# Optimization experiments

Hardware: AMD Instinct MI355X
Metric: run time of the kernel (lower is better)

The kernel has to match this reference:

```python
import jax, jax.numpy as jnp
import numpy as np

COST_CLASS = 1.0
COST_OBJECTNESS = 5.0
COST_GIOU = 2.0
COST_CENTER = 10.0

B, Q, G, C = 32, 1024, 64, 256


def _lsa(cost):
    """Exact rectangular linear sum assignment (Jonker-Volgenant shortest
    augmenting path, same algorithm as scipy.optimize.linear_sum_assignment).
    cost: (R, Cc) float64 numpy array. Returns (row_ind, col_ind), row_ind sorted."""
    transposed = cost.shape[0] > cost.shape[1]
    if transposed:
        cost = cost.T
    n, m = cost.shape
    u = np.zeros(n)
    v = np.zeros(m)
    col4row = np.full(n, -1, dtype=np.int64)
    row4col = np.full(m, -1, dtype=np.int64)
    for cur_row in range(n):
        shortest = np.full(m, np.inf)
        path = np.full(m, -1, dtype=np.int64)
        SC = np.zeros(m, dtype=bool)
        SR_rows = []
        min_val = 0.0
        i = cur_row
        sink = -1
        while sink == -1:
            SR_rows.append(i)
            idx = np.where(~SC)[0]
            r = min_val + cost[i, idx] - u[i] - v[idx]
            better = r < shortest[idx]
            upd = idx[better]
            shortest[upd] = r[better]
            path[upd] = i
            j = idx[np.argmin(shortest[idx])]
            min_val = shortest[j]
            SC[j] = True
            if row4col[j] == -1:
                sink = j
            else:
                i = row4col[j]
        # dual variable update
        u[cur_row] += min_val
        for irow in SR_rows:
            if irow != cur_row:
                u[irow] += min_val - shortest[col4row[irow]]
        v[SC] -= min_val - shortest[SC]
        # augment along the alternating path back to cur_row
        j = sink
        while True:
            i = path[j]
            row4col[j] = i
            col4row[i], j = j, col4row[i]
            if i == cur_row:
                break
    if transposed:
        order = np.argsort(col4row)
        return col4row[order], np.arange(n)[order]
    return np.arange(n), col4row


def setup_inputs() -> dict:
    key = jax.random.key(0)
    k1, k2, k3, k4, k5 = jax.random.split(key, 5)
    return {
        "sem_cls_prob": jax.random.uniform(k1, (B, Q, C), dtype=jnp.float32),
        "objectness_prob": jax.random.uniform(k2, (B, Q), dtype=jnp.float32),
        "center_dist": jax.random.uniform(k3, (B, Q, G), dtype=jnp.float32),
        "gious": jax.random.uniform(k4, (B, Q, G), dtype=jnp.float32),
        "nactual_gt": jax.random.randint(k5, (B,), 0, G, dtype=jnp.int64)
        if jax.config.jax_enable_x64 else jax.random.randint(k5, (B,), 0, G).astype(jnp.int32),
    }


def reference(sem_cls_prob, objectness_prob, center_dist, gious, nactual_gt):
    batchsize, nprop = objectness_prob.shape
    # class_mat == 0 in the original module
    final_cost = (COST_OBJECTNESS * (-objectness_prob[..., None])
                  + COST_CENTER * center_dist
                  + COST_GIOU * (-gious))  # [B, Q, G]
    cost_np = np.asarray(final_cost, dtype=np.float64)
    ngt = np.asarray(nactual_gt)
    per_prop_gt_inds = np.zeros((batchsize, nprop), dtype=np.int64)
    proposal_matched_mask = np.zeros((batchsize, nprop), dtype=np.float32)
    for b in range(batchsize):  # per-batch independent Hungarian (as in source)
        g = int(ngt[b])
        if g > 0:
            rows, cols = _lsa(cost_np[b, :, :g])
            per_prop_gt_inds[b, rows] = cols
            proposal_matched_mask[b, rows] = 1.0
    return jnp.asarray(per_prop_gt_inds), jnp.asarray(proposal_matched_mask)
```

## Files before the change

kernel.cpp:

```cpp
#include <hip/hip_runtime.h>
#include <math.h>

#define B_ 32
#define Q_ 1024
#define G_ 64
#define K16 16

typedef double v16d __attribute__((ext_vector_type(16)));
typedef float  v16f __attribute__((ext_vector_type(16)));
typedef int    v16i __attribute__((ext_vector_type(16)));

#define REP16(OP) OP(0,0) OP(1,1) OP(2,2) OP(3,3) OP(4,4) OP(5,5) OP(6,6) OP(7,7) \
                  OP(8,8) OP(9,9) OP(10,a) OP(11,b) OP(12,c) OP(13,d) OP(14,e) OP(15,f)
#define REP16A(OP,A) OP(A,0,0) OP(A,1,1) OP(A,2,2) OP(A,3,3) OP(A,4,4) OP(A,5,5) OP(A,6,6) OP(A,7,7) \
                     OP(A,8,8) OP(A,9,9) OP(A,10,a) OP(A,11,b) OP(A,12,c) OP(A,13,d) OP(A,14,e) OP(A,15,f)

#define ROR1 0x121
#define ROR2 0x122
#define ROR4 0x124
#define ROR8 0x128
#define BC15 0x142
#define BC31 0x143

template<int CTRL>
__device__ __forceinline__ double dpp_f64(double x) {
    union { double d; int i[2]; } a; a.d = x;
    union { int i[2]; double d; } r;
    r.i[0] = __builtin_amdgcn_update_dpp(a.i[0], a.i[0], CTRL, 0xF, 0xF, false);
    r.i[1] = __builtin_amdgcn_update_dpp(a.i[1], a.i[1], CTRL, 0xF, 0xF, false);
    return r.d;
}
template<int CTRL>
__device__ __forceinline__ int dpp_i32(int x) {
    return __builtin_amdgcn_update_dpp(x, x, CTRL, 0xF, 0xF, false);
}

__device__ __forceinline__ double readlane_f64(double x, int sl) {
    const int s = __builtin_amdgcn_readfirstlane(sl);
    union { double d; int i2[2]; } a; a.d = x;
    union { int i2[2]; double d; } r;
    r.i2[0] = __builtin_amdgcn_readlane(a.i2[0], s);
    r.i2[1] = __builtin_amdgcn_readlane(a.i2[1], s);
    return r.d;
}
__device__ __forceinline__ double readlane_f64c(double x, int sl) {
    union { double d; int i2[2]; } a; a.d = x;
    union { int i2[2]; double d; } r;
    r.i2[0] = __builtin_amdgcn_readlane(a.i2[0], sl);
    r.i2[1] = __builtin_amdgcn_readlane(a.i2[1], sl);
    return r.d;
}
__device__ __forceinline__ float readlane_f32u(float x, int sl) {
    union { float f; int i; } a; a.f = x;
    union { int i; float f; } r;
    r.i = __builtin_amdgcn_readlane(a.i, __builtin_amdgcn_readfirstlane(sl));
    return r.f;
}
__device__ __forceinline__ int readlane_i32(int x, int sl) {
    return __builtin_amdgcn_readlane(x, __builtin_amdgcn_readfirstlane(sl));
}
__device__ __forceinline__ int readlane_i32c(int x, int sl) {
    return __builtin_amdgcn_readlane(x, sl);
}

__device__ __forceinline__ int sel16v(v16i p, int s) {
    const int t0_0 = (s & 1) ? p.s1 : p.s0;
    const int t0_1 = (s & 1) ? p.s3 : p.s2;
    const int t0_2 = (s & 1) ? p.s5 : p.s4;
    const int t0_3 = (s & 1) ? p.s7 : p.s6;
    const int t0_4 = (s & 1) ? p.s9 : p.s8;
    const int t0_5 = (s & 1) ? p.sb : p.sa;
    const int t0_6 = (s & 1) ? p.sd : p.sc;
    const int t0_7 = (s & 1) ? p.sf : p.se;
    const int t1_0 = (s & 2) ? t0_1 : t0_0;
    const int t1_1 = (s & 2) ? t0_3 : t0_2;
    const int t1_2 = (s & 2) ? t0_5 : t0_4;
    const int t1_3 = (s & 2) ? t0_7 : t0_6;
    const int a0 = (s & 4) ? t1_1 : t1_0;
    const int a1 = (s & 4) ? t1_3 : t1_2;
    return (s & 8) ? a1 : a0;
}
__device__ __forceinline__ v16i set_el16(v16i v, int idx, bool cond, int val) {
#define SE16_(K,H) v.s##H = (cond && idx == K) ? val : v.s##H;
    REP16(SE16_)
#undef SE16_
    return v;
}

__device__ __forceinline__ void lexpair(v16d cand, int l,
                                        double& gv_o, int& jm_o) {
    double v = cand.s0; int j = l;
#define LPK_(K,H) if (K > 0) { const bool t = cand.s##H < v; \
    v = t ? cand.s##H : v; j = t ? (l + (K << 6)) : j; }
    REP16(LPK_)
#undef LPK_
#define LP_STEP(C) { const double pv = dpp_f64<C>(v); const int pj = dpp_i32<C>(j); \
    const bool t = (pv < v) || ((pv == v) && (pj < j)); \
    v = t ? pv : v; j = t ? pj : j; }
    LP_STEP(ROR1) LP_STEP(ROR2) LP_STEP(ROR4) LP_STEP(ROR8)
    LP_STEP(BC15) LP_STEP(BC31)
#undef LP_STEP
    gv_o = readlane_f64c(v, 63);
    jm_o = readlane_i32c(j, 63);
}

__global__ __launch_bounds__(256) void build_kernel(
    const float* __restrict__ obj, const float* __restrict__ cd,
    const float* __restrict__ gi, float* __restrict__ ct,
    float* __restrict__ pv, int* __restrict__ pj)
{
    __shared__ float tile[64][65];
    const int b  = blockIdx.y;
    const int jb = blockIdx.x << 6;
    const int t  = threadIdx.x;
    const float* objb = obj + (b << 10);
    const float4* cd4 = (const float4*)(cd + ((size_t)b << 16));
    const float4* gi4 = (const float4*)(gi + ((size_t)b << 16));

    #pragma unroll
    for (int p = 0; p < 4; ++p) {
        const int f  = t + (p << 8);
        const int jj = f >> 4;
        const int q  = f & 15;
        const int i0 = q << 2;
        const int j  = jb + jj;
        const float om = __fmul_rn(5.0f, -objb[j]);
        const float4 c4 = cd4[(j << 4) + q];
        const float4 q4 = gi4[(j << 4) + q];
        tile[i0 + 0][jj] = __fadd_rn(__fadd_rn(om, __fmul_rn(10.0f, c4.x)), __fmul_rn(2.0f, -q4.x));
        tile[i0 + 1][jj] = __fadd_rn(__fadd_rn(om, __fmul_rn(10.0f, c4.y)), __fmul_rn(2.0f, -q4.y));
        tile[i0 + 2][jj] = __fadd_rn(__fadd_rn(om, __fmul_rn(10.0f, c4.z)), __fmul_rn(2.0f, -q4.z));
        tile[i0 + 3][jj] = __fadd_rn(__fadd_rn(om, __fmul_rn(10.0f, c4.w)), __fmul_rn(2.0f, -q4.w));
    }
    __syncthreads();
    #pragma unroll
    for (int r = 0; r < 16; ++r) {
        const int idx = (r << 8) + t;
        const int i = idx >> 6, j2 = idx & 63;
        ct[(((size_t)(b << 6) + i) << 10) + jb + j2] = tile[i][j2];
    }
    if (t < 64) {
        float bv = tile[t][0]; int bc = 0;
        #pragma unroll 8
        for (int c = 1; c < 64; ++c) {
            const float v = tile[t][c];
            if (v < bv) { bv = v; bc = c; }
        }
        const int o = (((b << 6) + t) << 4) + blockIdx.x;
        pv[o] = bv;
        pj[o] = jb + bc;
    }
}

#define LD_W_(D,K,H) D.s##H = rp_[(K) << 6];
#define LD_N_(D,K,H) { const int idx_ = ((l + ((K) << 6)) << 6) + ri_; \
    D.s##H = __fadd_rn(__fadd_rn(objm.s##H, __fmul_rn(10.0f, cdb[idx_])), \
                       __fmul_rn(2.0f, -gib[idx_])); }
#define LOAD_ROW(ri, dst) { const int ri_ = (ri); \
    if (HASWS) { const float* rp_ = ctb + ((size_t)ri_ << 10) + l; REP16A(LD_W_, dst) } \
    else       { REP16A(LD_N_, dst) } }

template<bool HASWS>
__global__ __launch_bounds__(64, 1) void matcher_k(
    const float* __restrict__ obj, const float* __restrict__ cd,
    const float* __restrict__ gi, const int* __restrict__ ngt,
    const float* __restrict__ ct, const float* __restrict__ pv,
    const int* __restrict__ pj, float* __restrict__ out_ind,
    float* __restrict__ out_mask)
{
    const int b = blockIdx.x;
    const int l = threadIdx.x;
    const int g = ngt[b];

    const float* objb = obj + (b << 10);
    const float* cdb  = cd + ((size_t)b << 16);
    const float* gib  = gi + ((size_t)b << 16);
    const float* ctb  = HASWS ? (ct + ((size_t)(b << 6) << 10)) : (const float*)nullptr;

    v16f objm;
    if (!HASWS) {
#define OBJI_(K,H) objm.s##H = __fmul_rn(5.0f, -objb[l + (K << 6)]);
        REP16(OBJI_)
#undef OBJI_
    }

    float pre_v = 0.0f; int pre_j = 0;
    if (HASWS) {
        const float* pvb = pv + (((b << 6) + l) << 4);
        const int*   pjb = pj + (((b << 6) + l) << 4);
        float bv = pvb[0]; int bj = pjb[0];
        #pragma unroll
        for (int q = 1; q < 16; ++q) {
            const float vq = pvb[q];
            const int  jq = pjb[q];
            if (vq < bv) { bv = vq; bj = jq; }
        }
        pre_v = bv; pre_j = bj;
    } else if (g > 0) {
        for (int i = 0; i < g; ++i) {
            v16f c; LOAD_ROW(i, c)
            v16d c64;
#define CV_(K,H) c64.s##H = (double)c.s##H;
            REP16(CV_)
#undef CV_
            double gv; int j0;
            lexpair(c64, l, gv, j0);
            pre_v = (l == i) ? (float)gv : pre_v;
            pre_j = (l == i) ? j0 : pre_j;
        }
    }

    const double INF = __builtin_inf();
    double u_rep = 0.0;
    double m_rec = 0.0;
    bool   inSR  = false;
    int    c4r_rep = -1;
    unsigned asg   = 0u;
    unsigned dirty = 0u;
    v16d v_r, sh_r;
    v16i path, r4c;
    v16f c_cur, c_i;
#define INI_(K,H) { v_r.s##H = 0.0; sh_r.s##H = 0.0; path.s##H = 0; r4c.s##H = -1; }
    REP16(INI_)
#undef INI_

    for (int cur = 0; cur < g; ++cur) {
        double minv = (double)readlane_f32u(pre_v, cur);
        int jm = readlane_i32(pre_j, cur);
        const unsigned dw = (unsigned)readlane_i32((int)dirty, jm & 63);
        bool have_cur = false;
        if ((dw >> (jm >> 6)) & 1u) {
            LOAD_ROW(cur, c_cur) have_cur = true;
            v16d rr0;
#define RR0_(K,H) rr0.s##H = (double)c_cur.s##H - v_r.s##H;
            REP16(RR0_)
#undef RR0_
            lexpair(rr0, l, minv, jm);
        }
        const int owner0 = jm & 63, slot0 = jm >> 6;
        const unsigned oa0 = (unsigned)readlane_i32((int)asg, owner0);

        if (!((oa0 >> slot0) & 1u)) {
            u_rep   = (l == cur)    ? u_rep + minv : u_rep;
            c4r_rep = (l == cur)    ? jm           : c4r_rep;
            asg     = (l == owner0) ? (asg | (1u << slot0)) : asg;
            r4c     = set_el16(r4c, slot0, l == owner0, cur);
        } else {
            if (!have_cur) LOAD_ROW(cur, c_cur)
            int i = readlane_i32(sel16v(r4c, slot0), owner0);
            double ui = readlane_f64(u_rep, i);
            LOAD_ROW(i, c_i)
            unsigned sc = (l == owner0) ? (1u << slot0) : 0u;
            inSR  = (l == i);
            m_rec = minv;
#define SH0_(K,H) { sh_r.s##H = (double)c_cur.s##H - v_r.s##H; path.s##H = cur; }
            REP16(SH0_)
#undef SH0_

            int sink = -1;
            while (sink < 0) {
                v16d cand;
#define DST_(K,H) { const double rr = ((minv + (double)c_i.s##H) - ui) - v_r.s##H; \
                    const bool notSC = !((sc >> K) & 1u); \
                    const bool upd = notSC && (rr < sh_r.s##H);  \
                    sh_r.s##H = upd ? rr : sh_r.s##H; \
                    path.s##H = upd ? i : path.s##H; \
                    cand.s##H = notSC ? sh_r.s##H : INF; }
                REP16(DST_)
#undef DST_
                lexpair(cand, l, minv, jm);
                const int ow = jm & 63, sl = jm >> 6;
                if (l == ow) sc |= (1u << sl);
                const int insp = readlane_i32(sel16v(r4c, sl), ow);
                const unsigned oa = (unsigned)readlane_i32((int)asg, ow);
                if (!((oa >> sl) & 1u)) {
                    sink = jm;
                } else {
                    i = insp;
                    if (l == i) { inSR = true; m_rec = minv; }
                    ui = readlane_f64(u_rep, i);
                    LOAD_ROW(i, c_i)
                }
            }

            if (l == cur)       u_rep += minv;
            else if (inSR)      u_rep += minv - m_rec;
#define VUP_(K,H) { const double nv = v_r.s##H - (minv - sh_r.s##H); \
                    v_r.s##H = ((sc >> K) & 1u) ? nv : v_r.s##H; }
            REP16(VUP_)
#undef VUP_
            dirty |= sc;

            int j = sink;
            while (true) {
                const int so = j & 63, ss = j >> 6;
                const int ii = readlane_i32(sel16v(path, ss), so);
                const int nj = readlane_i32(c4r_rep, ii);
                r4c     = set_el16(r4c, ss, l == so, ii);
                asg     = (l == so) ? (asg | (1u << ss)) : asg;
                c4r_rep = (l == ii) ? j : c4r_rep;
                j = nj;
                if (ii == cur) break;
            }
        }
    }

#define OUT_(K,H) { const int rc = r4c.s##H; const int jj = l + (K << 6); \
    out_ind [(b << 10) + jj] = (rc >= 0) ? (float)rc : 0.0f; \
    out_mask[(b << 10) + jj] = (rc >= 0) ? 1.0f : 0.0f; }
    REP16(OUT_)
#undef OUT_
}

extern "C" void kernel_launch(void* const* d_in, const int* in_sizes, int n_in,
                              void* d_out, int out_size, void* d_ws, size_t ws_size,
                              hipStream_t stream)
{
    const float* obj = (const float*)d_in[1];
    const float* cd  = (const float*)d_in[2];
    const float* gi  = (const float*)d_in[3];
    const int*   ngt = (const int*)d_in[4];
    float* out0 = (float*)d_out;
    float* out1 = out0 + B_ * Q_;

    const size_t ct_b = (size_t)B_ * G_ * Q_ * sizeof(float);
    const size_t pv_b = (size_t)B_ * G_ * 16 * sizeof(float);
    if (ws_size >= ct_b + 2 * pv_b) {
        float* ct = (float*)d_ws;
        float* pv = (float*)((char*)d_ws + ct_b);
        int*   pj = (int*)((char*)d_ws + ct_b + pv_b);
        build_kernel<<<dim3(16, B_), 256, 0, stream>>>(obj, cd, gi, ct, pv, pj);
        matcher_k<true><<<B_, 64, 0, stream>>>(obj, cd, gi, ngt, ct, pv, pj, out0, out1);
    } else {
        matcher_k<false><<<B_, 64, 0, stream>>>(obj, cd, gi, ngt,
                                                nullptr, nullptr, nullptr, out0, out1);
    }
}
```

Measured before the change: 177.4 us.

## Add second-best column precompute, ballot-based assignment lookup, and cheaper argmin reduction

The build kernel now also tracks the second-smallest cost per row, and the matcher merges both. When the best column has been modified, the second-best is used to skip reloading and rescanning the row, as long as it is still clean. The dirty mask now only marks columns whose dual actually changed. The r4c vector is removed in favour of a wave ballot over col4row. Lexpair is rewritten as a value-only DPP min followed by a packed-key index min, which shortens the reduction chain on every Dijkstra step. The risks are subtle correctness issues in tie-breaking and the second-best shortcut, plus extra workspace traffic.

```diff
diff --git a/kernel.cpp b/kernel.cpp
--- a/kernel.cpp
+++ b/kernel.cpp
@@ -63,7 +63,7 @@
     return __builtin_amdgcn_readlane(x, sl);
 }
 
-__device__ __forceinline__ int sel16v(v16i p, int s) {
+__device__ __forceinline__ int sel16v_i(v16i p, int s) {
     const int t0_0 = (s & 1) ? p.s1 : p.s0;
     const int t0_1 = (s & 1) ? p.s3 : p.s2;
     const int t0_2 = (s & 1) ? p.s5 : p.s4;
@@ -80,34 +80,61 @@
     const int a1 = (s & 4) ? t1_3 : t1_2;
     return (s & 8) ? a1 : a0;
 }
-__device__ __forceinline__ v16i set_el16(v16i v, int idx, bool cond, int val) {
-#define SE16_(K,H) v.s##H = (cond && idx == K) ? val : v.s##H;
-    REP16(SE16_)
-#undef SE16_
-    return v;
-}
-
-__device__ __forceinline__ void lexpair(v16d cand, int l,
+__device__ __forceinline__ double sel16v_d(v16d p, int s) {
+    const double t0_0 = (s & 1) ? p.s1 : p.s0;
+    const double t0_1 = (s & 1) ? p.s3 : p.s2;
+    const double t0_2 = (s & 1) ? p.s5 : p.s4;
+    const double t0_3 = (s & 1) ? p.s7 : p.s6;
+    const double t0_4 = (s & 1) ? p.s9 : p.s8;
+    const double t0_5 = (s & 1) ? p.sb : p.sa;
+    const double t0_6 = (s & 1) ? p.sd : p.sc;
+    const double t0_7 = (s & 1) ? p.sf : p.se;
+    const double t1_0 = (s & 2) ? t0_1 : t0_0;
+    const double t1_1 = (s & 2) ? t0_3 : t0_2;
+    const double t1_2 = (s & 2) ? t0_5 : t0_4;
+    const double t1_3 = (s & 2) ? t0_7 : t0_6;
+    const double a0 = (s & 4) ? t1_1 : t1_0;
+    const double a1 = (s & 4) ? t1_3 : t1_2;
+    return (s & 8) ? a1 : a0;
+}
+
+__device__ __forceinline__ void lexpair(v16d c, int l,
                                         double& gv_o, int& jm_o) {
-    double v = cand.s0; int j = l;
-#define LPK_(K,H) if (K > 0) { const bool t = cand.s##H < v; \
-    v = t ? cand.s##H : v; j = t ? (l + (K << 6)) : j; }
-    REP16(LPK_)
-#undef LPK_
-#define LP_STEP(C) { const double pv = dpp_f64<C>(v); const int pj = dpp_i32<C>(j); \
-    const bool t = (pv < v) || ((pv == v) && (pj < j)); \
-    v = t ? pv : v; j = t ? pj : j; }
-    LP_STEP(ROR1) LP_STEP(ROR2) LP_STEP(ROR4) LP_STEP(ROR8)
-    LP_STEP(BC15) LP_STEP(BC31)
-#undef LP_STEP
-    gv_o = readlane_f64c(v, 63);
-    jm_o = readlane_i32c(j, 63);
+    const double a0 = fmin(c.s0, c.s1), a1 = fmin(c.s2, c.s3),
+                 a2 = fmin(c.s4, c.s5), a3 = fmin(c.s6, c.s7),
+                 a4 = fmin(c.s8, c.s9), a5 = fmin(c.sa, c.sb),
+                 a6 = fmin(c.sc, c.sd), a7 = fmin(c.se, c.sf);
+    const double b0 = fmin(a0, a1), b1 = fmin(a2, a3),
+                 b2 = fmin(a4, a5), b3 = fmin(a6, a7);
+    const double d0 = fmin(b0, b1), d1 = fmin(b2, b3);
+    const double vloc = fmin(d0, d1);
+    double v = vloc;
+#define VS_(C) { const double pv = dpp_f64<C>(v); v = fmin(pv, v); }
+    VS_(ROR1) VS_(ROR2) VS_(ROR4) VS_(ROR8) VS_(BC15) VS_(BC31)
+#undef VS_
+    const double gv = readlane_f64c(v, 63);
+    const int bit3 = (d0 == gv) ? 0 : 1;
+    const double bsel = bit3 ? b2 : b0;
+    const int bit2 = (bsel == gv) ? 0 : 1;
+    const double asel = bit2 ? (bit3 ? a6 : a2) : (bit3 ? a4 : a0);
+    const int bit1 = (asel == gv) ? 0 : 1;
+    const double csel = bit1 ? (bit2 ? (bit3 ? c.se : c.s6) : (bit3 ? c.sa : c.s2))
+                             : (bit2 ? (bit3 ? c.sc : c.s4) : (bit3 ? c.s8 : c.s0));
+    const int bit0 = (csel == gv) ? 0 : 1;
+    const int kloc = (bit3 << 3) | (bit2 << 2) | (bit1 << 1) | bit0;
+    int key = (vloc == gv) ? ((kloc << 6) | l) : 0x7FFFFFFF;
+#define KS_(C) { const int pk = dpp_i32<C>(key); key = (pk < key) ? pk : key; }
+    KS_(ROR1) KS_(ROR2) KS_(ROR4) KS_(ROR8) KS_(BC15) KS_(BC31)
+#undef KS_
+    jm_o = readlane_i32c(key, 63);
+    gv_o = gv;
 }
 
 __global__ __launch_bounds__(256) void build_kernel(
     const float* __restrict__ obj, const float* __restrict__ cd,
     const float* __restrict__ gi, float* __restrict__ ct,
-    float* __restrict__ pv, int* __restrict__ pj)
+    float* __restrict__ pv, int* __restrict__ pj,
+    float* __restrict__ pv2, int* __restrict__ pj2)
 {
     __shared__ float tile[64][65];
     const int b  = blockIdx.y;
@@ -141,14 +168,20 @@
     }
     if (t < 64) {
         float bv = tile[t][0]; int bc = 0;
+        float sv = 1e30f;      int sc2 = 0;
         #pragma unroll 8
         for (int c = 1; c < 64; ++c) {
             const float v = tile[t][c];
-            if (v < bv) { bv = v; bc = c; }
+            const bool t1 = v < bv;
+            const bool t2 = (!t1) && (v < sv);
+            sv  = t1 ? bv : (t2 ? v : sv);
+            sc2 = t1 ? bc : (t2 ? c : sc2);
+            bv  = t1 ? v : bv;
+            bc  = t1 ? c : bc;
         }
         const int o = (((b << 6) + t) << 4) + blockIdx.x;
-        pv[o] = bv;
-        pj[o] = jb + bc;
+        pv[o]  = bv;  pj[o]  = jb + bc;
+        pv2[o] = sv;  pj2[o] = jb + sc2;
     }
 }
 
@@ -165,7 +198,8 @@
     const float* __restrict__ obj, const float* __restrict__ cd,
     const float* __restrict__ gi, const int* __restrict__ ngt,
     const float* __restrict__ ct, const float* __restrict__ pv,
-    const int* __restrict__ pj, float* __restrict__ out_ind,
+    const int* __restrict__ pj, const float* __restrict__ pv2,
+    const int* __restrict__ pj2, float* __restrict__ out_ind,
     float* __restrict__ out_mask)
 {
     const int b = blockIdx.x;
@@ -184,18 +218,29 @@
 #undef OBJI_
     }
 
-    float pre_v = 0.0f; int pre_j = 0;
+    float pre_v = 0.0f, sec_v = 0.0f; int pre_j = 0, sec_j = 0;
     if (HASWS) {
-        const float* pvb = pv + (((b << 6) + l) << 4);
-        const int*   pjb = pj + (((b << 6) + l) << 4);
-        float bv = pvb[0]; int bj = pjb[0];
-        #pragma unroll
-        for (int q = 1; q < 16; ++q) {
-            const float vq = pvb[q];
-            const int  jq = pjb[q];
-            if (vq < bv) { bv = vq; bj = jq; }
-        }
-        pre_v = bv; pre_j = bj;
+        const int base = ((b << 6) + l) << 4;
+        const float4* pvq = (const float4*)(pv  + base);
+        const int4*   pjq = (const int4*)(pj  + base);
+        const float4* svq = (const float4*)(pv2 + base);
+        const int4*   sjq = (const int4*)(pj2 + base);
+        const float4 pA = pvq[0], pB = pvq[1], pC = pvq[2], pD = pvq[3];
+        const int4   jA = pjq[0], jB = pjq[1], jC = pjq[2], jD = pjq[3];
+        const float4 sA = svq[0], sB = svq[1], sC = svq[2], sD = svq[3];
+        const int4   tA = sjq[0], tB = sjq[1], tC = sjq[2], tD = sjq[3];
+        float bv = pA.x; int bj = jA.x; float sv = sA.x; int sj = tA.x;
+#define MERGE_(CV,CJ,C2V,C2J) { const bool nb = (CV) < bv; \
+    const bool s1 = (C2V) < bv; const bool s2 = (CV) < sv; \
+    const float nsv = nb ? (s1 ? (C2V) : bv) : (s2 ? (CV) : sv); \
+    const int   nsj = nb ? (s1 ? (C2J) : bj) : (s2 ? (CJ) : sj); \
+    bj = nb ? (CJ) : bj; bv = nb ? (CV) : bv; sv = nsv; sj = nsj; }
+        MERGE_(pA.y,jA.y,sA.y,tA.y) MERGE_(pA.z,jA.z,sA.z,tA.z) MERGE_(pA.w,jA.w,sA.w,tA.w)
+        MERGE_(pB.x,jB.x,sB.x,tB.x) MERGE_(pB.y,jB.y,sB.y,tB.y) MERGE_(pB.z,jB.z,sB.z,tB.z) MERGE_(pB.w,jB.w,sB.w,tB.w)
+        MERGE_(pC.x,jC.x,sC.x,tC.x) MERGE_(pC.y,jC.y,sC.y,tC.y) MERGE_(pC.z,jC.z,sC.z,tC.z) MERGE_(pC.w,jC.w,sC.w,tC.w)
+        MERGE_(pD.x,jD.x,sD.x,tD.x) MERGE_(pD.y,jD.y,sD.y,tD.y) MERGE_(pD.z,jD.z,sD.z,tD.z) MERGE_(pD.w,jD.w,sD.w,tD.w)
+#undef MERGE_
+        pre_v = bv; pre_j = bj; sec_v = sv; sec_j = sj;
     } else if (g > 0) {
         for (int i = 0; i < g; ++i) {
             v16f c; LOAD_ROW(i, c)
@@ -208,6 +253,7 @@
             pre_v = (l == i) ? (float)gv : pre_v;
             pre_j = (l == i) ? j0 : pre_j;
         }
+        sec_v = pre_v; sec_j = pre_j;
     }
 
     const double INF = __builtin_inf();
@@ -218,39 +264,53 @@
     unsigned asg   = 0u;
     unsigned dirty = 0u;
     v16d v_r, sh_r;
-    v16i path, r4c;
+    v16i path;
     v16f c_cur, c_i;
-#define INI_(K,H) { v_r.s##H = 0.0; sh_r.s##H = 0.0; path.s##H = 0; r4c.s##H = -1; }
+#define INI_(K,H) { v_r.s##H = 0.0; sh_r.s##H = 0.0; path.s##H = 0; }
     REP16(INI_)
 #undef INI_
 
     for (int cur = 0; cur < g; ++cur) {
-        double minv = (double)readlane_f32u(pre_v, cur);
+        const float pre_vc = readlane_f32u(pre_v, cur);
         int jm = readlane_i32(pre_j, cur);
-        const unsigned dw = (unsigned)readlane_i32((int)dirty, jm & 63);
+        double minv = (double)pre_vc;
         bool have_cur = false;
-        if ((dw >> (jm >> 6)) & 1u) {
-            LOAD_ROW(cur, c_cur) have_cur = true;
-            v16d rr0;
+        {
+            const int ow1 = jm & 63, sl1 = jm >> 6;
+            const unsigned d1 = (unsigned)readlane_i32((int)dirty, ow1);
+            if ((d1 >> sl1) & 1u) {
+                const float sv_c = readlane_f32u(sec_v, cur);
+                const int   sj_c = readlane_i32(sec_j, cur);
+                const unsigned d2 = (unsigned)readlane_i32((int)dirty, sj_c & 63);
+                if (!((d2 >> (sj_c >> 6)) & 1u)) {
+                    const double vpj = readlane_f64(sel16v_d(v_r, sl1), ow1);
+                    const double vA = (double)pre_vc - vpj;
+                    const double vB = (double)sv_c;
+                    const bool t = (vB < vA) || ((vB == vA) && (sj_c < jm));
+                    minv = t ? vB : vA;
+                    jm   = t ? sj_c : jm;
+                } else {
+                    LOAD_ROW(cur, c_cur) have_cur = true;
+                    v16d rr0;
 #define RR0_(K,H) rr0.s##H = (double)c_cur.s##H - v_r.s##H;
-            REP16(RR0_)
+                    REP16(RR0_)
 #undef RR0_
-            lexpair(rr0, l, minv, jm);
+                    lexpair(rr0, l, minv, jm);
+                }
+            }
         }
-        const int owner0 = jm & 63, slot0 = jm >> 6;
-        const unsigned oa0 = (unsigned)readlane_i32((int)asg, owner0);
-
-        if (!((oa0 >> slot0) & 1u)) {
-            u_rep   = (l == cur)    ? u_rep + minv : u_rep;
-            c4r_rep = (l == cur)    ? jm           : c4r_rep;
-            asg     = (l == owner0) ? (asg | (1u << slot0)) : asg;
-            r4c     = set_el16(r4c, slot0, l == owner0, cur);
+        const unsigned long long mk0 = __ballot(c4r_rep == jm);
+
+        if (mk0 == 0ull) {
+            u_rep   = (l == cur) ? u_rep + minv : u_rep;
+            c4r_rep = (l == cur) ? jm           : c4r_rep;
+            asg     = (l == (jm & 63)) ? (asg | (1u << (jm >> 6))) : asg;
         } else {
             if (!have_cur) LOAD_ROW(cur, c_cur)
-            int i = readlane_i32(sel16v(r4c, slot0), owner0);
+            int i = (int)__builtin_ctzll(mk0);
+            LOAD_ROW(i, c_i)
             double ui = readlane_f64(u_rep, i);
-            LOAD_ROW(i, c_i)
-            unsigned sc = (l == owner0) ? (1u << slot0) : 0u;
+            unsigned sc = (l == (jm & 63)) ? (1u << (jm >> 6)) : 0u;
             inSR  = (l == i);
             m_rec = minv;
 #define SH0_(K,H) { sh_r.s##H = (double)c_cur.s##H - v_r.s##H; path.s##H = cur; }
@@ -269,34 +329,34 @@
                 REP16(DST_)
 #undef DST_
                 lexpair(cand, l, minv, jm);
-                const int ow = jm & 63, sl = jm >> 6;
-                if (l == ow) sc |= (1u << sl);
-                const int insp = readlane_i32(sel16v(r4c, sl), ow);
-                const unsigned oa = (unsigned)readlane_i32((int)asg, ow);
-                if (!((oa >> sl) & 1u)) {
+                const unsigned long long mk = __ballot(c4r_rep == jm);
+                if (l == (jm & 63)) sc |= (1u << (jm >> 6));
+                if (mk == 0ull) {
                     sink = jm;
                 } else {
-                    i = insp;
+                    i = (int)__builtin_ctzll(mk);
+                    LOAD_ROW(i, c_i)
                     if (l == i) { inSR = true; m_rec = minv; }
                     ui = readlane_f64(u_rep, i);
-                    LOAD_ROW(i, c_i)
                 }
             }
 
             if (l == cur)       u_rep += minv;
             else if (inSR)      u_rep += minv - m_rec;
-#define VUP_(K,H) { const double nv = v_r.s##H - (minv - sh_r.s##H); \
-                    v_r.s##H = ((sc >> K) & 1u) ? nv : v_r.s##H; }
+            unsigned chg = 0u;
+#define VUP_(K,H) { const bool in_sc = (sc >> K) & 1u; \
+                    const double nv = v_r.s##H - (minv - sh_r.s##H); \
+                    chg = (in_sc && (sh_r.s##H != minv)) ? (chg | (1u << K)) : chg; \
+                    v_r.s##H = in_sc ? nv : v_r.s##H; }
             REP16(VUP_)
 #undef VUP_
-            dirty |= sc;
+            dirty |= chg;
 
             int j = sink;
             while (true) {
                 const int so = j & 63, ss = j >> 6;
-                const int ii = readlane_i32(sel16v(path, ss), so);
+                const int ii = readlane_i32(sel16v_i(path, ss), so);
                 const int nj = readlane_i32(c4r_rep, ii);
-                r4c     = set_el16(r4c, ss, l == so, ii);
                 asg     = (l == so) ? (asg | (1u << ss)) : asg;
                 c4r_rep = (l == ii) ? j : c4r_rep;
                 j = nj;
@@ -305,11 +365,12 @@
         }
     }
 
-#define OUT_(K,H) { const int rc = r4c.s##H; const int jj = l + (K << 6); \
-    out_ind [(b << 10) + jj] = (rc >= 0) ? (float)rc : 0.0f; \
-    out_mask[(b << 10) + jj] = (rc >= 0) ? 1.0f : 0.0f; }
+#define OUT_(K,H) { const int jj = l + (K << 6); const bool a_ = (asg >> K) & 1u; \
+    out_mask[(b << 10) + jj] = a_ ? 1.0f : 0.0f; \
+    if (!a_) out_ind[(b << 10) + jj] = 0.0f; }
     REP16(OUT_)
 #undef OUT_
+    if (c4r_rep >= 0) out_ind[(b << 10) + c4r_rep] = (float)l;
 }
 
 extern "C" void kernel_launch(void* const* d_in, const int* in_sizes, int n_in,
@@ -325,14 +386,17 @@
 
     const size_t ct_b = (size_t)B_ * G_ * Q_ * sizeof(float);
     const size_t pv_b = (size_t)B_ * G_ * 16 * sizeof(float);
-    if (ws_size >= ct_b + 2 * pv_b) {
-        float* ct = (float*)d_ws;
-        float* pv = (float*)((char*)d_ws + ct_b);
-        int*   pj = (int*)((char*)d_ws + ct_b + pv_b);
-        build_kernel<<<dim3(16, B_), 256, 0, stream>>>(obj, cd, gi, ct, pv, pj);
-        matcher_k<true><<<B_, 64, 0, stream>>>(obj, cd, gi, ngt, ct, pv, pj, out0, out1);
+    if (ws_size >= ct_b + 4 * pv_b) {
+        float* ct  = (float*)d_ws;
+        float* pv  = (float*)((char*)d_ws + ct_b);
+        int*   pj  = (int*)  ((char*)d_ws + ct_b + pv_b);
+        float* pv2 = (float*)((char*)d_ws + ct_b + 2 * pv_b);
+        int*   pj2 = (int*)  ((char*)d_ws + ct_b + 3 * pv_b);
+        build_kernel<<<dim3(16, B_), 256, 0, stream>>>(obj, cd, gi, ct, pv, pj, pv2, pj2);
+        matcher_k<true><<<B_, 64, 0, stream>>>(obj, cd, gi, ngt, ct, pv, pj, pv2, pj2,
+                                               out0, out1);
     } else {
-        matcher_k<false><<<B_, 64, 0, stream>>>(obj, cd, gi, ngt,
+        matcher_k<false><<<B_, 64, 0, stream>>>(obj, cd, gi, ngt, nullptr, nullptr,
                                                 nullptr, nullptr, nullptr, out0, out1);
     }
 }
```

Result: faster. 160.2 us (-9.7%).
